# Optimization experiments

Hardware: AMD Instinct MI355X
Metric: run time of the kernel (lower is better)

Reference implementation:

```python
import jax, jax.numpy as jnp
import numpy as np

B, S, D = 2, 2048, 1024   # batch, seq, hidden_dim
I = 512                   # intermediate_dim (per-expert FFN width)
E = 16                    # num_experts
TOP_K = 2


def setup_inputs() -> dict:
    key = jax.random.key(0)
    ks = jax.random.split(key, 10)
    sc_d = 1.0 / np.sqrt(D)
    sc_i = 1.0 / np.sqrt(I)
    return {
        "x": jax.random.normal(ks[0], (B, S, D), dtype=jnp.float32),
        # router gate: Linear(D -> E) with bias (nnx.Linear default)
        "gate_w": jax.random.normal(ks[1], (D, E), dtype=jnp.float32) * sc_d,
        "gate_b": jnp.zeros((E,), dtype=jnp.float32),
        # shared expert MLP (SwiGLU: down(silu(gate(x)) * up(x)))
        "shared_wg": jax.random.normal(ks[2], (D, I), dtype=jnp.float32) * sc_d,
        "shared_wu": jax.random.normal(ks[3], (D, I), dtype=jnp.float32) * sc_d,
        "shared_wd": jax.random.normal(ks[4], (I, D), dtype=jnp.float32) * sc_i,
        # routed experts, stacked on leading E axis
        "experts_wg": jax.random.normal(ks[5], (E, D, I), dtype=jnp.float32) * sc_d,
        "experts_wu": jax.random.normal(ks[6], (E, D, I), dtype=jnp.float32) * sc_d,
        "experts_wd": jax.random.normal(ks[7], (E, I, D), dtype=jnp.float32) * sc_i,
    }


def _mlp(x, wg, wu, wd):
    # SwiGLU MLP: down(silu(gate(x)) * up(x))
    return jnp.einsum("bsi,id->bsd", jax.nn.silu(x @ wg) * (x @ wu), wd)


def reference(x, gate_w, gate_b, shared_wg, shared_wu, shared_wd,
              experts_wg, experts_wu, experts_wd):
    # router: sigmoid logits -> top_k -> normalize by sum of selected scores
    router_logits = jax.nn.sigmoid(x @ gate_w + gate_b)          # [B,S,E]
    expert_values, expert_indices = jax.lax.top_k(router_logits, k=TOP_K)
    expert_values = expert_values / jnp.sum(expert_values, axis=-1, keepdims=True)

    # dense all-expert compute (faithful to source): [B,S,E,D]
    hg = jnp.einsum("bsd,edi->bsei", x, experts_wg)
    hu = jnp.einsum("bsd,edi->bsei", x, experts_wu)
    all_outputs = jnp.einsum("bsei,eid->bsed", jax.nn.silu(hg) * hu, experts_wd)

    # gather top-k expert outputs: [B,S,K,D]
    selected = jnp.take_along_axis(all_outputs, expert_indices[..., None], axis=2)
    expert_weighted = jnp.sum(expert_values[..., None] * selected, axis=2)  # [B,S,D]

    return x + _mlp(x, shared_wg, shared_wu, shared_wd) + expert_weighted
```

## Files before the change

kernel.cpp:

```cpp
#include <hip/hip_runtime.h>
#include <stdint.h>

typedef __attribute__((ext_vector_type(8))) short short8;
typedef __attribute__((ext_vector_type(4))) float f32x4;

#define TOKENS 4096
#define DDIM 1024
#define IDIM 512
#define NEXP 16
#define NEXP1 17
#define CSTRIDE 32

#define OFF_WGU   0ull
#define OFF_WD    35651584ull
#define OFF_XB    53477376ull
#define OFF_HGU   61865984ull
#define OFF_H     87031808ull
#define OFF_TOK   99614720ull
#define OFF_REC   99893248ull
#define OFF_WREC  99926016ull
#define OFF_CNT   100171776ull
#define OFF_BASE  100175872ull

__device__ __forceinline__ float bf2f(unsigned short u) {
    union { uint32_t i; float f; } v; v.i = ((uint32_t)u) << 16; return v.f;
}
__device__ __forceinline__ unsigned short f2bf(float f) {
    union { float f; uint32_t i; } v; v.f = f;
    uint32_t r = v.i + 0x7FFFu + ((v.i >> 16) & 1u);
    return (unsigned short)(r >> 16);
}
__device__ __forceinline__ void cp16(const unsigned short* g, unsigned short* l) {
    __builtin_amdgcn_global_load_lds(
        (const __attribute__((address_space(1))) uint32_t*)g,
        (__attribute__((address_space(3))) uint32_t*)l, 16, 0, 0);
}

__global__ __launch_bounds__(256)
void k_transpose(const float* __restrict__ eg, const float* __restrict__ eu,
                 const float* __restrict__ ed, const float* __restrict__ sg,
                 const float* __restrict__ su, const float* __restrict__ sd,
                 unsigned short* __restrict__ Wgu, unsigned short* __restrict__ Wd)
{
    int z = blockIdx.z;
    int e = z / 3, m = z % 3;
    int R = (m == 2) ? 512 : 1024;
    int C = (m == 2) ? 1024 : 512;
    int r0 = blockIdx.y * 64, c0 = blockIdx.x * 64;
    if (r0 >= R || c0 >= C) return;
    const float* src;
    if (m == 0)      src = (e < 16) ? eg + (size_t)e * 524288 : sg;
    else if (m == 1) src = (e < 16) ? eu + (size_t)e * 524288 : su;
    else             src = (e < 16) ? ed + (size_t)e * 524288 : sd;

    __shared__ float tl[64 * 65];
    const int tid = threadIdx.x;

    {
        const int lr = tid >> 4;
        const int lc = (tid & 15) * 4;
        #pragma unroll
        for (int ps = 0; ps < 4; ++ps) {
            int r = ps * 16 + lr;
            float4 v = *(const float4*)(src + (size_t)(r0 + r) * C + (c0 + lc));
            float* d = &tl[r * 65 + lc];
            d[0] = v.x; d[1] = v.y; d[2] = v.z; d[3] = v.w;
        }
    }
    __syncthreads();

    {
        const int nl = tid >> 2;
        const int kc = (tid & 3) * 16;
        unsigned short ov[16];
        #pragma unroll
        for (int j = 0; j < 16; ++j)
            ov[j] = f2bf(tl[(kc + j) * 65 + nl]);
        int n = c0 + nl;
        int k = r0 + kc;
        unsigned short* dst;
        if (m < 2) dst = Wgu + (size_t)e * 1048576 + (size_t)(n + (m == 1 ? 512 : 0)) * 1024 + k;
        else       dst = Wd  + (size_t)e * 524288  + (size_t)n * 512 + k;
        *(uint4*)dst       = *(uint4*)&ov[0];
        *(uint4*)(dst + 8) = *(uint4*)&ov[8];
    }
}

__global__ void k_xconv(const float* __restrict__ x, unsigned short* __restrict__ xb,
                        int* __restrict__ tok)
{
    int i = blockIdx.x * 256 + threadIdx.x;
    float4 v = ((const float4*)x)[i];
    ushort4 b;
    b.x = f2bf(v.x); b.y = f2bf(v.y); b.z = f2bf(v.z); b.w = f2bf(v.w);
    ((ushort4*)xb)[i] = b;
    if (i < TOKENS) tok[16 * 4096 + i] = i;
}

__global__ __launch_bounds__(512, 4)
void k_router(const float* __restrict__ x, const float* __restrict__ gw,
              const float* __restrict__ gb, int* __restrict__ tok,
              int2* __restrict__ rec, float2* __restrict__ wrec,
              int* __restrict__ counts)
{
    __shared__ float gws[1024 * 12];

    const int t = blockIdx.x * 8 + (threadIdx.x >> 6);
    const int lane = threadIdx.x & 63;
    const float* xr = x + (size_t)t * DDIM;

    float xv[16];
    #pragma unroll
    for (int kk = 0; kk < 16; ++kk) xv[kk] = xr[kk * 64 + lane];

    float v[16];

    for (int p = 0; p < 2; ++p) {
        __syncthreads();
        #pragma unroll
        for (int c = 0; c < 4; ++c) {
            int idx = threadIdx.x + c * 512;
            int k = idx >> 1;
            int h = (idx & 1) * 4;
            float4 g4 = *(const float4*)(gw + k * 16 + p * 8 + h);
            *(float4*)&gws[k * 12 + h] = g4;
        }
        __syncthreads();

        double a[8];
        #pragma unroll
        for (int j = 0; j < 8; ++j) a[j] = 0.0;

        #pragma unroll
        for (int kk = 0; kk < 16; ++kk) {
            int kl = kk * 64 + lane;
            float4 gA = *(const float4*)&gws[kl * 12];
            float4 gB = *(const float4*)&gws[kl * 12 + 4];
            double xd = (double)xv[kk];
            a[0] += xd * (double)gA.x; a[1] += xd * (double)gA.y;
            a[2] += xd * (double)gA.z; a[3] += xd * (double)gA.w;
            a[4] += xd * (double)gB.x; a[5] += xd * (double)gB.y;
            a[6] += xd * (double)gB.z; a[7] += xd * (double)gB.w;
        }

        #pragma unroll
        for (int off = 32; off > 0; off >>= 1) {
            #pragma unroll
            for (int j = 0; j < 8; ++j)
                a[j] += __shfl_xor(a[j], off, 64);
        }

        #pragma unroll
        for (int j = 0; j < 8; ++j)
            v[p * 8 + j] = 1.0f / (1.0f + expf(-(float)(a[j] + (double)gb[p * 8 + j])));
    }

    if (lane == 0) {
        int i0 = 0;
        #pragma unroll
        for (int e = 1; e < 16; ++e) if (v[e] > v[i0]) i0 = e;
        int i1 = (i0 == 0) ? 1 : 0;
        #pragma unroll
        for (int e = 0; e < 16; ++e) if (e != i0 && e != i1 && v[e] > v[i1]) i1 = e;
        float s = v[i0] + v[i1];
        float w0 = v[i0] / s, w1 = v[i1] / s;
        int p0 = atomicAdd(&counts[i0 * CSTRIDE], 1);
        tok[i0 * 4096 + p0] = t;
        int p1 = atomicAdd(&counts[i1 * CSTRIDE], 1);
        tok[i1 * 4096 + p1] = t;
        rec[t]  = make_int2(i0 * 4096 + p0, i1 * 4096 + p1);
        wrec[t] = make_float2(w0, w1);
    }
}

__global__ void k_prefix(int* counts, int* bases)
{
    if (threadIdx.x == 0 && blockIdx.x == 0) {
        counts[16 * CSTRIDE] = TOKENS;
        int a = 0;
        for (int e = 0; e < NEXP1; ++e) { bases[e] = a; a += counts[e * CSTRIDE]; }
        bases[17] = a;
    }
}

template <int MODE>
__global__ __launch_bounds__(256, 3)
void k_gemm(const unsigned short* __restrict__ Amat, const unsigned short* __restrict__ Bmat,
            const int* __restrict__ tok, const int* __restrict__ counts,
            const int* __restrict__ bases, unsigned short* __restrict__ Hgu)
{
    constexpr int K = (MODE == 0) ? 1024 : 512;
    const int e = blockIdx.z;
    const int cnt = counts[e * CSTRIDE];
    const int m0 = blockIdx.y * 128;
    if (m0 >= cnt) return;
    const int n0 = blockIdx.x * 128;
    const int base = bases[e];

    __shared__ unsigned short As[128 * 32];
    __shared__ unsigned short Bs[128 * 32];

    const int tid  = threadIdx.x;
    const int wave = tid >> 6;
    const int lane = tid & 63;
    const int lrow = lane >> 2;
    const int lseg = lane & 3;

    unsigned short* a_dst0 = &As[wave * 1024];
    unsigned short* a_dst1 = &As[wave * 1024 + 512];
    unsigned short* b_dst0 = &Bs[wave * 1024];
    unsigned short* b_dst1 = &Bs[wave * 1024 + 512];

    int ar0 = m0 + wave * 32 + lrow;      if (ar0 > cnt - 1) ar0 = cnt - 1;
    int ar1 = m0 + wave * 32 + 16 + lrow; if (ar1 > cnt - 1) ar1 = cnt - 1;
    size_t ai0, ai1;
    if (MODE == 0) { ai0 = (size_t)tok[e * 4096 + ar0]; ai1 = (size_t)tok[e * 4096 + ar1]; }
    else           { ai0 = (size_t)(base + ar0);        ai1 = (size_t)(base + ar1); }
    const unsigned short* ag0 = Amat + ai0 * K + lseg * 8;
    const unsigned short* ag1 = Amat + ai1 * K + lseg * 8;
    const size_t eoff = (size_t)e * 1024 * K;
    const unsigned short* bg0 = Bmat + eoff + (size_t)(n0 + wave * 32 + lrow) * K + lseg * 8;
    const unsigned short* bg1 = Bmat + eoff + (size_t)(n0 + wave * 32 + 16 + lrow) * K + lseg * 8;

    const int wm = wave & 1, wn = wave >> 1;
    const int q = lane >> 4, mc = lane & 15;

    f32x4 acc[4][4];
    #pragma unroll
    for (int i = 0; i < 4; ++i)
        #pragma unroll
        for (int j = 0; j < 4; ++j) acc[i][j] = (f32x4){0.f, 0.f, 0.f, 0.f};

    for (int k0 = 0; k0 < K; k0 += 32) {
        __syncthreads();
        cp16(ag0 + k0, a_dst0);
        cp16(ag1 + k0, a_dst1);
        cp16(bg0 + k0, b_dst0);
        cp16(bg1 + k0, b_dst1);
        __syncthreads();
        short8 a[4], b[4];
        #pragma unroll
        for (int i = 0; i < 4; ++i)
            a[i] = *(const short8*)&As[(wm * 64 + i * 16 + mc) * 32 + q * 8];
        #pragma unroll
        for (int j = 0; j < 4; ++j)
            b[j] = *(const short8*)&Bs[(wn * 64 + j * 16 + mc) * 32 + q * 8];
        #pragma unroll
        for (int i = 0; i < 4; ++i)
            #pragma unroll
            for (int j = 0; j < 4; ++j)
                acc[i][j] = __builtin_amdgcn_mfma_f32_16x16x32_bf16(a[i], b[j], acc[i][j], 0, 0, 0);
    }

    #pragma unroll
    for (int i = 0; i < 4; ++i) {
        int lr = wm * 64 + i * 16 + q * 4;
        #pragma unroll
        for (int r = 0; r < 4; ++r) {
            int mrow = m0 + lr + r;
            if (mrow >= cnt) continue;
            size_t rowoff = (size_t)(base + mrow) * 1024;
            #pragma unroll
            for (int j = 0; j < 4; ++j) {
                int gc = n0 + wn * 64 + j * 16 + mc;
                Hgu[rowoff + gc] = f2bf(acc[i][j][r]);
            }
        }
    }
}

__global__ void k_silu(const unsigned short* __restrict__ Hgu, unsigned short* __restrict__ H)
{
    int gid = blockIdx.x * 256 + threadIdx.x;
    int s = gid >> 6;
    int c = (gid & 63) * 8;
    const unsigned short* g = Hgu + (size_t)s * 1024 + c;
    unsigned short gg[8], uu[8], oo[8];
    *(uint4*)gg = *(const uint4*)g;
    *(uint4*)uu = *(const uint4*)(g + 512);
    #pragma unroll
    for (int j = 0; j < 8; ++j) {
        float gv = bf2f(gg[j]);
        float uv = bf2f(uu[j]);
        float sv = gv / (1.0f + __expf(-gv));
        oo[j] = f2bf(sv * uv);
    }
    *(uint4*)(H + (size_t)s * 512 + c) = *(uint4*)oo;
}

__global__ void k_combine(const float* __restrict__ x, const unsigned short* __restrict__ Hs,
                          const int2* __restrict__ rec, const float2* __restrict__ wrec,
                          const int* __restrict__ bases, float* __restrict__ out)
{
    int t = blockIdx.x * 2 + (threadIdx.x >> 7);
    int c = (threadIdx.x & 127) * 8;
    int2 r = rec[t];
    float2 w = wrec[t];
    int s0 = bases[r.x >> 12] + (r.x & 4095);
    int s1 = bases[r.y >> 12] + (r.y & 4095);
    int ss = 8192 + t;

    unsigned short h0[8], h1[8], hs[8];
    *(uint4*)h0 = *(const uint4*)(Hs + (size_t)s0 * 1024 + c);
    *(uint4*)h1 = *(const uint4*)(Hs + (size_t)s1 * 1024 + c);
    *(uint4*)hs = *(const uint4*)(Hs + (size_t)ss * 1024 + c);
    const float* xr = x + (size_t)t * 1024 + c;
    float o[8];
    #pragma unroll
    for (int j = 0; j < 8; ++j)
        o[j] = xr[j] + bf2f(hs[j]) + w.x * bf2f(h0[j]) + w.y * bf2f(h1[j]);
    float* orow = out + (size_t)t * 1024 + c;
    *(float4*)orow       = *(float4*)&o[0];
    *(float4*)(orow + 4) = *(float4*)&o[4];
}

extern "C" void kernel_launch(void* const* d_in, const int* in_sizes, int n_in,
                              void* d_out, int out_size, void* d_ws, size_t ws_size,
                              hipStream_t stream)
{
    const float* x  = (const float*)d_in[0];
    const float* gw = (const float*)d_in[1];
    const float* gb = (const float*)d_in[2];
    const float* sg = (const float*)d_in[3];
    const float* su = (const float*)d_in[4];
    const float* sd = (const float*)d_in[5];
    const float* eg = (const float*)d_in[6];
    const float* eu = (const float*)d_in[7];
    const float* ed = (const float*)d_in[8];
    float* out = (float*)d_out;
    char* ws = (char*)d_ws;

    unsigned short* Wgu = (unsigned short*)(ws + OFF_WGU);
    unsigned short* Wd  = (unsigned short*)(ws + OFF_WD);
    unsigned short* xb  = (unsigned short*)(ws + OFF_XB);
    unsigned short* Hgu = (unsigned short*)(ws + OFF_HGU);
    unsigned short* H   = (unsigned short*)(ws + OFF_H);
    int*    tok   = (int*)(ws + OFF_TOK);
    int2*   rec   = (int2*)(ws + OFF_REC);
    float2* wrec  = (float2*)(ws + OFF_WREC);
    int*    counts= (int*)(ws + OFF_CNT);
    int*    bases = (int*)(ws + OFF_BASE);

    hipMemsetAsync(counts, 0, 4096, stream);
    k_transpose<<<dim3(16, 16, 51), 256, 0, stream>>>(eg, eu, ed, sg, su, sd, Wgu, Wd);
    k_xconv<<<4096, 256, 0, stream>>>(x, xb, tok);
    k_router<<<512, 512, 0, stream>>>(x, gw, gb, tok, rec, wrec, counts);
    k_prefix<<<1, 64, 0, stream>>>(counts, bases);
    k_gemm<0><<<dim3(8, 32, 17), 256, 0, stream>>>(xb, Wgu, tok, counts, bases, Hgu);
    k_silu<<<3072, 256, 0, stream>>>(Hgu, H);
    k_gemm<1><<<dim3(8, 32, 17), 256, 0, stream>>>(H, Wd, tok, counts, bases, Hgu);
    k_combine<<<2048, 256, 0, stream>>>(x, Hgu, rec, wrec, bases, out);
}
```

Measured before the change: 292.7 us.

## Fuse SiLU gating into first GEMM epilogue and compact expert tile grid

Gate and up weight rows are interleaved so each GEMM output tile holds matching gate/up columns, letting the epilogue compute silu(g)*u through a lane shuffle and write H directly. This removes the separate SiLU kernel and the round-trip of the 2x-wide Hgu intermediate through memory. The grid is also flattened to a compact list of (expert, m-block) pairs built by the prefix kernel, which avoids launching many blocks that exit immediately. The trade-offs are a linear search for the expert in each block and a MAXMB cap of 112 m-blocks, which must cover the worst-case sum of tiles across experts.

```diff
diff --git a/kernel.cpp b/kernel.cpp
--- a/kernel.cpp
+++ b/kernel.cpp
@@ -10,6 +10,7 @@
 #define NEXP 16
 #define NEXP1 17
 #define CSTRIDE 32
+#define MAXMB 112
 
 #define OFF_WGU   0ull
 #define OFF_WD    35651584ull
@@ -79,7 +80,7 @@
         int n = c0 + nl;
         int k = r0 + kc;
         unsigned short* dst;
-        if (m < 2) dst = Wgu + (size_t)e * 1048576 + (size_t)(n + (m == 1 ? 512 : 0)) * 1024 + k;
+        if (m < 2) dst = Wgu + (size_t)e * 1048576 + (size_t)(2 * n + m) * 1024 + k;
         else       dst = Wd  + (size_t)e * 524288  + (size_t)n * 512 + k;
         *(uint4*)dst       = *(uint4*)&ov[0];
         *(uint4*)(dst + 8) = *(uint4*)&ov[8];
@@ -173,13 +174,18 @@
     }
 }
 
-__global__ void k_prefix(int* counts, int* bases)
+__global__ void k_prefix(int* counts, int* bases, int* mbp)
 {
     if (threadIdx.x == 0 && blockIdx.x == 0) {
         counts[16 * CSTRIDE] = TOKENS;
-        int a = 0;
-        for (int e = 0; e < NEXP1; ++e) { bases[e] = a; a += counts[e * CSTRIDE]; }
+        int a = 0, b = 0;
+        for (int e = 0; e < NEXP1; ++e) {
+            int c = counts[e * CSTRIDE];
+            bases[e] = a; a += c;
+            mbp[e] = b;  b += (c + 127) >> 7;
+        }
         bases[17] = a;
+        mbp[17] = b;
     }
 }
 
@@ -187,13 +193,16 @@
 __global__ __launch_bounds__(256, 3)
 void k_gemm(const unsigned short* __restrict__ Amat, const unsigned short* __restrict__ Bmat,
             const int* __restrict__ tok, const int* __restrict__ counts,
-            const int* __restrict__ bases, unsigned short* __restrict__ Hgu)
+            const int* __restrict__ bases, const int* __restrict__ mbp,
+            unsigned short* __restrict__ Out)
 {
     constexpr int K = (MODE == 0) ? 1024 : 512;
-    const int e = blockIdx.z;
+    const int my = blockIdx.y;
+    if (my >= mbp[17]) return;
+    int e = 0;
+    while (my >= mbp[e + 1]) ++e;
     const int cnt = counts[e * CSTRIDE];
-    const int m0 = blockIdx.y * 128;
-    if (m0 >= cnt) return;
+    const int m0 = (my - mbp[e]) * 128;
     const int n0 = blockIdx.x * 128;
     const int base = bases[e];
 
@@ -259,33 +268,23 @@
         for (int r = 0; r < 4; ++r) {
             int mrow = m0 + lr + r;
             if (mrow >= cnt) continue;
-            size_t rowoff = (size_t)(base + mrow) * 1024;
             #pragma unroll
             for (int j = 0; j < 4; ++j) {
                 int gc = n0 + wn * 64 + j * 16 + mc;
-                Hgu[rowoff + gc] = f2bf(acc[i][j][r]);
+                float val = acc[i][j][r];
+                if (MODE == 0) {
+                    float other = __shfl_xor(val, 1, 64);
+                    float g = (mc & 1) ? other : val;
+                    float u = (mc & 1) ? val : other;
+                    float h = g / (1.0f + __expf(-g)) * u;
+                    if ((mc & 1) == 0)
+                        Out[(size_t)(base + mrow) * 512 + (gc >> 1)] = f2bf(h);
+                } else {
+                    Out[(size_t)(base + mrow) * 1024 + gc] = f2bf(val);
+                }
             }
         }
     }
-}
-
-__global__ void k_silu(const unsigned short* __restrict__ Hgu, unsigned short* __restrict__ H)
-{
-    int gid = blockIdx.x * 256 + threadIdx.x;
-    int s = gid >> 6;
-    int c = (gid & 63) * 8;
-    const unsigned short* g = Hgu + (size_t)s * 1024 + c;
-    unsigned short gg[8], uu[8], oo[8];
-    *(uint4*)gg = *(const uint4*)g;
-    *(uint4*)uu = *(const uint4*)(g + 512);
-    #pragma unroll
-    for (int j = 0; j < 8; ++j) {
-        float gv = bf2f(gg[j]);
-        float uv = bf2f(uu[j]);
-        float sv = gv / (1.0f + __expf(-gv));
-        oo[j] = f2bf(sv * uv);
-    }
-    *(uint4*)(H + (size_t)s * 512 + c) = *(uint4*)oo;
 }
 
 __global__ void k_combine(const float* __restrict__ x, const unsigned short* __restrict__ Hs,
@@ -340,14 +339,14 @@
     float2* wrec  = (float2*)(ws + OFF_WREC);
     int*    counts= (int*)(ws + OFF_CNT);
     int*    bases = (int*)(ws + OFF_BASE);
+    int*    mbp   = bases + 20;
 
     hipMemsetAsync(counts, 0, 4096, stream);
     k_transpose<<<dim3(16, 16, 51), 256, 0, stream>>>(eg, eu, ed, sg, su, sd, Wgu, Wd);
     k_xconv<<<4096, 256, 0, stream>>>(x, xb, tok);
     k_router<<<512, 512, 0, stream>>>(x, gw, gb, tok, rec, wrec, counts);
-    k_prefix<<<1, 64, 0, stream>>>(counts, bases);
-    k_gemm<0><<<dim3(8, 32, 17), 256, 0, stream>>>(xb, Wgu, tok, counts, bases, Hgu);
-    k_silu<<<3072, 256, 0, stream>>>(Hgu, H);
-    k_gemm<1><<<dim3(8, 32, 17), 256, 0, stream>>>(H, Wd, tok, counts, bases, Hgu);
+    k_prefix<<<1, 64, 0, stream>>>(counts, bases, mbp);
+    k_gemm<0><<<dim3(8, MAXMB), 256, 0, stream>>>(xb, Wgu, tok, counts, bases, mbp, H);
+    k_gemm<1><<<dim3(8, MAXMB), 256, 0, stream>>>(H, Wd, tok, counts, bases, mbp, Hgu);
     k_combine<<<2048, 256, 0, stream>>>(x, Hgu, rec, wrec, bases, out);
 }
```

Result: no change. 288.9 us (-1.3%).
